# Kernel tuning notes

Hardware: AMD Instinct MI355X
Metric: run time of the kernel (lower is better)

The kernel has to match this reference:

```python
import jax, jax.numpy as jnp
import numpy as np

N = 2048
OUT = 16

def setup_inputs() -> dict:
    key = jax.random.key(0)
    k1, k2 = jax.random.split(key)
    inputs = jax.random.normal(k1, (N, N), dtype=jnp.float32)
    w = jax.random.normal(k2, (15, OUT), dtype=jnp.float32) * 0.05  # random_normal init
    return {"inputs": inputs, "w": w}

def reference(inputs, w):
    # inputs: [N, N], w: [15, out]
    n = inputs.shape[0]
    dt = inputs.dtype
    diag = jnp.diagonal(inputs)          # [N]
    rowsum = inputs.sum(axis=1)          # [N]  'ij->i'
    colsum = inputs.sum(axis=0)          # [N]  'ij->j'
    trace = diag.sum()
    totsum = inputs.sum()
    eye = jnp.eye(n, dtype=dt)
    ones = jnp.ones((n, n), dtype=dt)
    as_row = lambda v: jnp.broadcast_to(v[None, :], (n, n))  # ones_i * v_j -> ij
    as_col = lambda v: jnp.broadcast_to(v[:, None], (n, n))  # ones_i * v_j -> ji
    basis = jnp.stack([
        jnp.diag(diag),          # 0: diag embedded on diagonal
        jnp.diag(rowsum),        # 1
        jnp.diag(colsum),        # 2
        eye * trace,             # 3: identity * trace
        eye * totsum,            # 4: identity * totsum
        as_row(diag),            # 5: 'i,j->ij' ones, diag
        as_row(rowsum),          # 6
        as_row(colsum),          # 7
        as_col(diag),            # 8: 'i,j->ji' ones, diag
        as_col(rowsum),          # 9
        as_col(colsum),          # 10
        inputs.T,                # 11
        inputs,                  # 12
        ones * trace,            # 13
        ones * totsum,           # 14
    ], axis=-1)                  # [N, N, 15]
    # activation is identity (None)
    return jnp.einsum('ijk,ko->ijo', basis, w)  # [N, N, out]
```

## Files before the change

kernel.cpp:

```cpp
#include <hip/hip_runtime.h>

#define NMAT 2048

__device__ __forceinline__ float wave_reduce_sum(float v) {
    v += __shfl_down(v, 32);
    v += __shfl_down(v, 16);
    v += __shfl_down(v, 8);
    v += __shfl_down(v, 4);
    v += __shfl_down(v, 2);
    v += __shfl_down(v, 1);
    return v;
}

__device__ __forceinline__ float4 f4fma(float a, float4 b, float4 c) {
    return make_float4(fmaf(a, b.x, c.x), fmaf(a, b.y, c.y),
                       fmaf(a, b.z, c.z), fmaf(a, b.w, c.w));
}
__device__ __forceinline__ float4 f4scale(float a, float4 b) {
    return make_float4(a * b.x, a * b.y, a * b.z, a * b.w);
}

__global__ __launch_bounds__(256) void k_rows(const float* __restrict__ in,
                                              float* __restrict__ rowsum,
                                              float* __restrict__ diag,
                                              float* __restrict__ scal) {
    const int i = blockIdx.x;
    const float4* row = (const float4*)(in + (size_t)i * NMAT);
    float s = 0.f;
#pragma unroll
    for (int k = 0; k < 2; ++k) {
        float4 v = row[threadIdx.x + k * 256];
        s += (v.x + v.y) + (v.z + v.w);
    }
    s = wave_reduce_sum(s);
    __shared__ float red[4];
    const int lane = threadIdx.x & 63;
    const int wid = threadIdx.x >> 6;
    if (lane == 0) red[wid] = s;
    __syncthreads();
    if (threadIdx.x == 0) {
        float t = (red[0] + red[1]) + (red[2] + red[3]);
        rowsum[i] = t;
        atomicAdd(&scal[1], t);
        float d = in[(size_t)i * NMAT + i];
        diag[i] = d;
        atomicAdd(&scal[0], d);
    }
}

__global__ __launch_bounds__(256) void k_cols(const float* __restrict__ in,
                                              float* __restrict__ colsum) {
    const int j = blockIdx.x * 256 + threadIdx.x;
    const int r0 = blockIdx.y * 64;
    float s = 0.f;
#pragma unroll 8
    for (int r = 0; r < 64; ++r)
        s += in[(size_t)(r0 + r) * NMAT + j];
    atomicAdd(&colsum[j], s);
}

__global__ __launch_bounds__(256) void k_tables(const float* __restrict__ w,
                                                const float* __restrict__ rowsum,
                                                const float* __restrict__ diag,
                                                const float* __restrict__ colsum,
                                                const float* __restrict__ scal,
                                                float4* __restrict__ P4,
                                                float4* __restrict__ Q4,
                                                float4* __restrict__ D4) {
    const int idx = blockIdx.x * 256 + threadIdx.x;
    const int i = idx >> 2;
    const int og = idx & 3;
    const float di = diag[i], rs = rowsum[i], cs = colsum[i];
    const float tr = scal[0], ts = scal[1];
    const float4* W = (const float4*)w;
    float4 P = f4scale(di, W[8 * 4 + og]);
    P = f4fma(rs, W[9 * 4 + og], P);
    P = f4fma(cs, W[10 * 4 + og], P);
    P = f4fma(tr, W[13 * 4 + og], P);
    P = f4fma(ts, W[14 * 4 + og], P);
    float4 Q = f4scale(di, W[5 * 4 + og]);
    Q = f4fma(rs, W[6 * 4 + og], Q);
    Q = f4fma(cs, W[7 * 4 + og], Q);
    float4 D = f4scale(di, W[0 * 4 + og]);
    D = f4fma(rs, W[1 * 4 + og], D);
    D = f4fma(cs, W[2 * 4 + og], D);
    D = f4fma(tr, W[3 * 4 + og], D);
    D = f4fma(ts, W[4 * 4 + og], D);
    P4[idx] = P;
    Q4[idx] = Q;
    D4[idx] = D;
}

__global__ __launch_bounds__(256) void k_main(const float* __restrict__ in,
                                              const float* __restrict__ w,
                                              const float4* __restrict__ P4,
                                              const float4* __restrict__ Q4,
                                              const float4* __restrict__ D4,
                                              float4* __restrict__ out4) {
    const int t = threadIdx.x;
    const int og = t & 3;
    const int tj = (t >> 2) & 31;
    const int half = t >> 7;
    const int j = blockIdx.x * 32 + tj;
    const int i0 = blockIdx.y * 32;
    const float4* W = (const float4*)w;
    const float4 w11v = W[11 * 4 + og];
    const float4 w12v = W[12 * 4 + og];
    const float4 q = Q4[j * 4 + og];
    const size_t jrow = (size_t)j * NMAT;
#pragma unroll 4
    for (int it = 0; it < 16; ++it) {
        const int i = i0 + half + 2 * it;
        const float a = in[(size_t)i * NMAT + j];
        const float at = in[jrow + i];
        const float4 p = P4[i * 4 + og];
        float4 r;
        r.x = fmaf(a, w12v.x, fmaf(at, w11v.x, p.x + q.x));
        r.y = fmaf(a, w12v.y, fmaf(at, w11v.y, p.y + q.y));
        r.z = fmaf(a, w12v.z, fmaf(at, w11v.z, p.z + q.z));
        r.w = fmaf(a, w12v.w, fmaf(at, w11v.w, p.w + q.w));
        if (i == j) {
            const float4 dd = D4[i * 4 + og];
            r.x += dd.x; r.y += dd.y; r.z += dd.z; r.w += dd.w;
        }
        out4[((size_t)i * NMAT + j) * 4 + og] = r;
    }
}

extern "C" void kernel_launch(void* const* d_in, const int* in_sizes, int n_in,
                              void* d_out, int out_size, void* d_ws, size_t ws_size,
                              hipStream_t stream) {
    const float* in = (const float*)d_in[0];
    const float* w = (const float*)d_in[1];
    float* ws = (float*)d_ws;

    float* colsum = ws;
    float* scal = ws + 2048;
    float* rowsum = ws + 2056;
    float* diag = ws + 4104;
    float4* P4 = (float4*)(ws + 6152);
    float4* Q4 = (float4*)(ws + 6152 + 32768);
    float4* D4 = (float4*)(ws + 6152 + 65536);

    hipMemsetAsync(d_ws, 0, 2050 * sizeof(float), stream);
    k_rows<<<2048, 256, 0, stream>>>(in, rowsum, diag, scal);
    k_cols<<<dim3(8, 32), 256, 0, stream>>>(in, colsum);
    k_tables<<<32, 256, 0, stream>>>(w, rowsum, diag, colsum, scal, P4, Q4, D4);
    k_main<<<dim3(64, 64), 256, 0, stream>>>(in, w, P4, Q4, D4, (float4*)d_out);
}
```

Before: 349.6 us.

## Fuse row/col stats into one pass and compute tables inline in main kernel

Row sums, column sums and the diagonal are now gathered in a single kernel that reads each row once, instead of separate row and column kernels that each read the input. The per-row and per-column coefficient tables are no longer precomputed; the main kernel builds them from the statistics and the weights, computing the diagonal term only in diagonal blocks. Output is written with nontemporal stores and the loop is unrolled further. This removes two launches and an extra full read of the input, at the price of more arithmetic and more small loads per output element in the main kernel.

```diff
diff --git a/kernel.cpp b/kernel.cpp
--- a/kernel.cpp
+++ b/kernel.cpp
@@ -2,15 +2,7 @@
 
 #define NMAT 2048
 
-__device__ __forceinline__ float wave_reduce_sum(float v) {
-    v += __shfl_down(v, 32);
-    v += __shfl_down(v, 16);
-    v += __shfl_down(v, 8);
-    v += __shfl_down(v, 4);
-    v += __shfl_down(v, 2);
-    v += __shfl_down(v, 1);
-    return v;
-}
+typedef float f32x4 __attribute__((ext_vector_type(4)));
 
 __device__ __forceinline__ float4 f4fma(float a, float4 b, float4 c) {
     return make_float4(fmaf(a, b.x, c.x), fmaf(a, b.y, c.y),
@@ -20,82 +12,65 @@
     return make_float4(a * b.x, a * b.y, a * b.z, a * b.w);
 }
 
-__global__ __launch_bounds__(256) void k_rows(const float* __restrict__ in,
-                                              float* __restrict__ rowsum,
-                                              float* __restrict__ diag,
-                                              float* __restrict__ scal) {
-    const int i = blockIdx.x;
-    const float4* row = (const float4*)(in + (size_t)i * NMAT);
-    float s = 0.f;
+__global__ __launch_bounds__(256) void k_stats(const float* __restrict__ in,
+                                               float* __restrict__ rowsum,
+                                               float* __restrict__ diag,
+                                               float* __restrict__ colsum,
+                                               float* __restrict__ scal) {
+    const int t = threadIdx.x;
+    const int r0 = blockIdx.x * 8;
+    __shared__ float lrs[8][256];
+    float4 c0 = make_float4(0.f, 0.f, 0.f, 0.f);
+    float4 c1 = make_float4(0.f, 0.f, 0.f, 0.f);
 #pragma unroll
-    for (int k = 0; k < 2; ++k) {
-        float4 v = row[threadIdx.x + k * 256];
-        s += (v.x + v.y) + (v.z + v.w);
+    for (int r = 0; r < 8; ++r) {
+        const float4* row = (const float4*)(in + (size_t)(r0 + r) * NMAT);
+        float4 v0 = row[t];
+        float4 v1 = row[t + 256];
+        c0.x += v0.x; c0.y += v0.y; c0.z += v0.z; c0.w += v0.w;
+        c1.x += v1.x; c1.y += v1.y; c1.z += v1.z; c1.w += v1.w;
+        lrs[r][t] = ((v0.x + v0.y) + (v0.z + v0.w)) +
+                    ((v1.x + v1.y) + (v1.z + v1.w));
     }
-    s = wave_reduce_sum(s);
-    __shared__ float red[4];
-    const int lane = threadIdx.x & 63;
-    const int wid = threadIdx.x >> 6;
-    if (lane == 0) red[wid] = s;
+    atomicAdd(&colsum[4 * t + 0], c0.x);
+    atomicAdd(&colsum[4 * t + 1], c0.y);
+    atomicAdd(&colsum[4 * t + 2], c0.z);
+    atomicAdd(&colsum[4 * t + 3], c0.w);
+    atomicAdd(&colsum[1024 + 4 * t + 0], c1.x);
+    atomicAdd(&colsum[1024 + 4 * t + 1], c1.y);
+    atomicAdd(&colsum[1024 + 4 * t + 2], c1.z);
+    atomicAdd(&colsum[1024 + 4 * t + 3], c1.w);
     __syncthreads();
-    if (threadIdx.x == 0) {
-        float t = (red[0] + red[1]) + (red[2] + red[3]);
-        rowsum[i] = t;
-        atomicAdd(&scal[1], t);
-        float d = in[(size_t)i * NMAT + i];
-        diag[i] = d;
+    {
+        const int row = t >> 5;
+        const int lane = t & 31;
+        float s = 0.f;
+#pragma unroll
+        for (int k = 0; k < 8; ++k) s += lrs[row][lane + 32 * k];
+        s += __shfl_down(s, 16);
+        s += __shfl_down(s, 8);
+        s += __shfl_down(s, 4);
+        s += __shfl_down(s, 2);
+        s += __shfl_down(s, 1);
+        if (lane == 0) {
+            rowsum[r0 + row] = s;
+            atomicAdd(&scal[1], s);
+        }
+    }
+    if (t < 8) {
+        const int r = r0 + t;
+        const float d = in[(size_t)r * NMAT + r];
+        diag[r] = d;
         atomicAdd(&scal[0], d);
     }
 }
 
-__global__ __launch_bounds__(256) void k_cols(const float* __restrict__ in,
-                                              float* __restrict__ colsum) {
-    const int j = blockIdx.x * 256 + threadIdx.x;
-    const int r0 = blockIdx.y * 64;
-    float s = 0.f;
-#pragma unroll 8
-    for (int r = 0; r < 64; ++r)
-        s += in[(size_t)(r0 + r) * NMAT + j];
-    atomicAdd(&colsum[j], s);
-}
-
-__global__ __launch_bounds__(256) void k_tables(const float* __restrict__ w,
-                                                const float* __restrict__ rowsum,
-                                                const float* __restrict__ diag,
-                                                const float* __restrict__ colsum,
-                                                const float* __restrict__ scal,
-                                                float4* __restrict__ P4,
-                                                float4* __restrict__ Q4,
-                                                float4* __restrict__ D4) {
-    const int idx = blockIdx.x * 256 + threadIdx.x;
-    const int i = idx >> 2;
-    const int og = idx & 3;
-    const float di = diag[i], rs = rowsum[i], cs = colsum[i];
-    const float tr = scal[0], ts = scal[1];
-    const float4* W = (const float4*)w;
-    float4 P = f4scale(di, W[8 * 4 + og]);
-    P = f4fma(rs, W[9 * 4 + og], P);
-    P = f4fma(cs, W[10 * 4 + og], P);
-    P = f4fma(tr, W[13 * 4 + og], P);
-    P = f4fma(ts, W[14 * 4 + og], P);
-    float4 Q = f4scale(di, W[5 * 4 + og]);
-    Q = f4fma(rs, W[6 * 4 + og], Q);
-    Q = f4fma(cs, W[7 * 4 + og], Q);
-    float4 D = f4scale(di, W[0 * 4 + og]);
-    D = f4fma(rs, W[1 * 4 + og], D);
-    D = f4fma(cs, W[2 * 4 + og], D);
-    D = f4fma(tr, W[3 * 4 + og], D);
-    D = f4fma(ts, W[4 * 4 + og], D);
-    P4[idx] = P;
-    Q4[idx] = Q;
-    D4[idx] = D;
-}
-
 __global__ __launch_bounds__(256) void k_main(const float* __restrict__ in,
                                               const float* __restrict__ w,
-                                              const float4* __restrict__ P4,
-                                              const float4* __restrict__ Q4,
-                                              const float4* __restrict__ D4,
+                                              const float* __restrict__ rowsum,
+                                              const float* __restrict__ diag,
+                                              const float* __restrict__ colsum,
+                                              const float* __restrict__ scal,
                                               float4* __restrict__ out4) {
     const int t = threadIdx.x;
     const int og = t & 3;
@@ -103,27 +78,41 @@
     const int half = t >> 7;
     const int j = blockIdx.x * 32 + tj;
     const int i0 = blockIdx.y * 32;
+    const bool dblk = (blockIdx.x == blockIdx.y);
     const float4* W = (const float4*)w;
-    const float4 w11v = W[11 * 4 + og];
-    const float4 w12v = W[12 * 4 + og];
-    const float4 q = Q4[j * 4 + og];
+    const float4 w8 = W[8 * 4 + og], w9 = W[9 * 4 + og], w10 = W[10 * 4 + og];
+    const float4 w11 = W[11 * 4 + og], w12 = W[12 * 4 + og];
+    const float tr = scal[0], ts = scal[1];
+    float4 base = f4scale(diag[j], W[5 * 4 + og]);
+    base = f4fma(rowsum[j], W[6 * 4 + og], base);
+    base = f4fma(colsum[j], W[7 * 4 + og], base);
+    base = f4fma(tr, W[13 * 4 + og], base);
+    base = f4fma(ts, W[14 * 4 + og], base);
     const size_t jrow = (size_t)j * NMAT;
-#pragma unroll 4
+#pragma unroll 8
     for (int it = 0; it < 16; ++it) {
         const int i = i0 + half + 2 * it;
+        const float di = diag[i];
+        const float rsi = rowsum[i];
+        const float csi = colsum[i];
         const float a = in[(size_t)i * NMAT + j];
         const float at = in[jrow + i];
-        const float4 p = P4[i * 4 + og];
-        float4 r;
-        r.x = fmaf(a, w12v.x, fmaf(at, w11v.x, p.x + q.x));
-        r.y = fmaf(a, w12v.y, fmaf(at, w11v.y, p.y + q.y));
-        r.z = fmaf(a, w12v.z, fmaf(at, w11v.z, p.z + q.z));
-        r.w = fmaf(a, w12v.w, fmaf(at, w11v.w, p.w + q.w));
-        if (i == j) {
-            const float4 dd = D4[i * 4 + og];
+        float4 r = f4fma(di, w8, base);
+        r = f4fma(rsi, w9, r);
+        r = f4fma(csi, w10, r);
+        r = f4fma(a, w12, r);
+        r = f4fma(at, w11, r);
+        if (dblk && i == j) {
+            float4 dd = f4scale(di, W[0 * 4 + og]);
+            dd = f4fma(rsi, W[1 * 4 + og], dd);
+            dd = f4fma(csi, W[2 * 4 + og], dd);
+            dd = f4fma(tr, W[3 * 4 + og], dd);
+            dd = f4fma(ts, W[4 * 4 + og], dd);
             r.x += dd.x; r.y += dd.y; r.z += dd.z; r.w += dd.w;
         }
-        out4[((size_t)i * NMAT + j) * 4 + og] = r;
+        f32x4 rv = {r.x, r.y, r.z, r.w};
+        __builtin_nontemporal_store(
+            rv, (f32x4*)&out4[((size_t)i * NMAT + j) * 4 + og]);
     }
 }
 
@@ -138,13 +127,9 @@
     float* scal = ws + 2048;
     float* rowsum = ws + 2056;
     float* diag = ws + 4104;
-    float4* P4 = (float4*)(ws + 6152);
-    float4* Q4 = (float4*)(ws + 6152 + 32768);
-    float4* D4 = (float4*)(ws + 6152 + 65536);
 
     hipMemsetAsync(d_ws, 0, 2050 * sizeof(float), stream);
-    k_rows<<<2048, 256, 0, stream>>>(in, rowsum, diag, scal);
-    k_cols<<<dim3(8, 32), 256, 0, stream>>>(in, colsum);
-    k_tables<<<32, 256, 0, stream>>>(w, rowsum, diag, colsum, scal, P4, Q4, D4);
-    k_main<<<dim3(64, 64), 256, 0, stream>>>(in, w, P4, Q4, D4, (float4*)d_out);
+    k_stats<<<256, 256, 0, stream>>>(in, rowsum, diag, colsum, scal);
+    k_main<<<dim3(64, 64), 256, 0, stream>>>(in, w, rowsum, diag, colsum, scal,
+                                             (float4*)d_out);
 }
```

After: 311.5 us. 1.12x faster.
